# Performance work log

Hardware: AMD Instinct MI355X
Metric: run time of the kernel (lower is better)

## Reference

```python
import jax, jax.numpy as jnp
import numpy as np

N = 100_000            # nodes
E = 1_600_000          # edges per metapath
IN = 256               # input features
HEADS, DIM = 8, 16     # heads * dim = hidden_channels
HIDDEN = HEADS * DIM   # 128
OUT = 4                # classes
NEG_SLOPE = 0.2


def setup_inputs() -> dict:
    key = jax.random.key(0)
    ks = jax.random.split(key, 16)
    s = 1.0 / np.sqrt(HIDDEN)
    return {
        "x": jax.random.normal(ks[0], (N, IN), jnp.float32),
        "edge_index0": jax.random.randint(ks[1], (2, E), 0, N, jnp.int64),
        "edge_index1": jax.random.randint(ks[2], (2, E), 0, N, jnp.int64),
        "proj_w": jax.random.normal(ks[3], (IN, HIDDEN), jnp.float32) / np.sqrt(IN),
        "proj_b": jnp.zeros((HIDDEN,), jnp.float32),
        "att_src0": jax.random.normal(ks[4], (HEADS, DIM), jnp.float32) * s,
        "att_dst0": jax.random.normal(ks[5], (HEADS, DIM), jnp.float32) * s,
        "att_src1": jax.random.normal(ks[6], (HEADS, DIM), jnp.float32) * s,
        "att_dst1": jax.random.normal(ks[7], (HEADS, DIM), jnp.float32) * s,
        "k_lin_w": jax.random.normal(ks[8], (HIDDEN, HIDDEN), jnp.float32) * s,
        "k_lin_b": jnp.zeros((HIDDEN,), jnp.float32),
        "q": jax.random.normal(ks[9], (HIDDEN,), jnp.float32) * s,
        "lin_w": jax.random.normal(ks[10], (HIDDEN, OUT), jnp.float32) * s,
        "lin_b": jnp.zeros((OUT,), jnp.float32),
    }


def _metapath_conv(xp, a_src, a_dst, src, dst):
    # xp: [N,H,D]; a_src, a_dst: [H,D]; src/dst: [E]
    alpha_src = (xp * a_src).sum(-1)                     # [N,H]
    alpha_dst = (xp * a_dst).sum(-1)                     # [N,H]
    e = jax.nn.leaky_relu(alpha_src[src] + alpha_dst[dst], NEG_SLOPE)  # [E,H]
    emax = jax.ops.segment_max(e, dst, num_segments=N)  # [N,H] (stable softmax)
    e = jnp.exp(e - emax[dst])
    denom = jax.ops.segment_sum(e, dst, num_segments=N)
    alpha = e / (denom[dst] + 1e-16)                     # edge softmax per dst
    msg = xp[src] * alpha[..., None]                     # [E,H,D]
    out = jax.ops.segment_sum(msg, dst, num_segments=N)  # [N,H,D]
    return jax.nn.relu(out.reshape(N, HIDDEN))


def reference(x, edge_index0, edge_index1, proj_w, proj_b,
              att_src0, att_dst0, att_src1, att_dst1,
              k_lin_w, k_lin_b, q, lin_w, lin_b):
    # shared node-type projection
    xp = (x @ proj_w + proj_b).reshape(N, HEADS, DIM)
    # per-metapath GAT-style convolutions (dropout=0.6 is eval no-op)
    outs = jnp.stack([
        _metapath_conv(xp, att_src0, att_dst0, edge_index0[0], edge_index0[1]),
        _metapath_conv(xp, att_src1, att_dst1, edge_index1[0], edge_index1[1]),
    ])                                                    # [M,N,HIDDEN]
    # semantic attention over metapaths
    k = jnp.tanh(outs @ k_lin_w + k_lin_b).mean(axis=1)  # [M,HIDDEN]
    attn = jax.nn.softmax((k * q).sum(-1))               # [M]
    fused = (attn[:, None, None] * outs).sum(0)          # [N,HIDDEN]
    return fused @ lin_w + lin_b                          # [N,OUT]
```

## Files before the change

kernel.cpp:

```cpp
#include <hip/hip_runtime.h>
#include <hip/hip_bf16.h>

#define NN 100000
#define EE 1600000
#define HID 128
#define NEG 0.2f
#define CAP 64
#define BSH 9
#define NB 196
#define CAPB 9216
#define EBLK 4096
#define NBINB 391
#define NBUILD 392
#define NPROJ 512
#define NPREPW 208

typedef __attribute__((ext_vector_type(8))) short short8;
typedef __attribute__((ext_vector_type(4))) float f32x4;

static __device__ __forceinline__ float bf2f(short s) {
  union { float f; unsigned u; } c;
  c.u = ((unsigned)(unsigned short)s) << 16;
  return c.f;
}

static __device__ __forceinline__ float exp2_fast(float x) {
  float r;
  asm("v_exp_f32 %0, %1" : "=v"(r) : "v"(x));
  return r;
}

static __device__ __forceinline__ float tanh_fast(float x) {
  float a = fminf(fmaxf(x * 2.885390082f, -40.f), 40.f);
  float e = exp2_fast(a);
  float r = __builtin_amdgcn_rcpf(e + 1.f);
  return fmaf(-2.f, r, 1.f);
}

__global__ __launch_bounds__(256) void k_prep(const int* __restrict__ ei0,
    const int* __restrict__ ei1, const float* __restrict__ w,
    const float* __restrict__ kw,
    const float* __restrict__ a0s, const float* __restrict__ a0d,
    const float* __restrict__ a1s, const float* __restrict__ a1d,
    int* __restrict__ gcur, int* __restrict__ binned,
    short* __restrict__ wTg, short* __restrict__ kwTg, short* __restrict__ awTg) {
  const int bid = blockIdx.x;
  const int t = threadIdx.x;
  if (bid >= 2 * NBINB) {
    int i = (bid - 2 * NBINB) * 256 + t;
    if (i < 32768) {
      int n = i >> 8, k = i & 255;
      __hip_bfloat16 b = __float2bfloat16(w[k * 128 + n]);
      wTg[i] = *(short*)&b;
    } else if (i < 49152) {
      int j = i - 32768;
      int n = j >> 7, k = j & 127;
      __hip_bfloat16 b = __float2bfloat16(kw[k * 128 + n]);
      kwTg[j] = *(short*)&b;
    } else if (i < 53248) {
      int j = i - 49152;
      int c = j >> 7, k = j & 127;
      int p = c >> 4, dt = (c >> 3) & 1, h = c & 7;
      const float* arr = p ? (dt ? a1d : a1s) : (dt ? a0d : a0s);
      float v = ((k >> 4) == h) ? arr[h * 16 + (k & 15)] * 1.44269504f : 0.f;
      __hip_bfloat16 b = __float2bfloat16(v);
      awTg[j] = *(short*)&b;
    }
    return;
  }
  const int p = bid >= NBINB;
  const int bx = p ? bid - NBINB : bid;
  const int* __restrict__ ei = p ? ei1 : ei0;
  const int* __restrict__ src = ei;
  const int* __restrict__ dst = ei + EE;
  int* __restrict__ gc = gcur + p * 256;
  int* __restrict__ bn = binned + (size_t)p * NB * CAPB;
  __shared__ int cntL[NB], baseL[NB];
  const int e0 = bx * EBLK;
  const int e1 = min(e0 + EBLK, EE);
  for (int i = t; i < NB; i += 256) cntL[i] = 0;
  __syncthreads();
  int vj[16], bj[16];
#pragma unroll
  for (int j = 0; j < 16; j++) {
    int e = e0 + t + j * 256;
    bj[j] = -1;
    if (e < e1) {
      int d = dst[e];
      int b = d >> BSH;
      int off = atomicAdd(&cntL[b], 1);
      vj[j] = (src[e] << BSH) | (d & 511);
      bj[j] = (b << 14) | off;
    }
  }
  __syncthreads();
  for (int i = t; i < NB; i += 256) baseL[i] = atomicAdd(&gc[i], cntL[i]);
  __syncthreads();
#pragma unroll
  for (int j = 0; j < 16; j++) {
    if (bj[j] >= 0) {
      int b = bj[j] >> 14;
      int off = baseL[b] + (bj[j] & 16383);
      if (off < CAPB) bn[b * CAPB + off] = vj[j];
    }
  }
}

#define PWS 264
#define AWS 136
#define PNT ((NN + 15) / 16)

__global__ __launch_bounds__(512) void k_mid(
    const int* __restrict__ gcur, const int* __restrict__ binned,
    int* __restrict__ cnt, int* __restrict__ csr,
    const float* __restrict__ x, const short* __restrict__ wTg,
    const short* __restrict__ awTg, const float* __restrict__ bias,
    __hip_bfloat16* __restrict__ xph, float* __restrict__ alpha) {
  __shared__ short wT[128 * PWS];
  __shared__ short awT[32 * AWS];
  const int bid = blockIdx.x;
  const int tid = threadIdx.x;
  if (bid < NBUILD) {
    int* lc = (int*)wT;
    const int p = bid >= 196, b = p ? bid - 196 : bid;
    const int* __restrict__ bn = binned + (size_t)p * NB * CAPB + (size_t)b * CAPB;
    const int n = min(gcur[p * 256 + b], CAPB);
    int* __restrict__ cs = csr + (size_t)p * NN * CAP;
    lc[tid] = 0;
    __syncthreads();
    const int node0 = b << BSH;
    for (int i = tid; i < n; i += 512) {
      int v = bn[i];
      int ln = v & 511;
      int off = atomicAdd(&lc[ln], 1);
      if (off < CAP) cs[(size_t)(node0 + ln) * CAP + off] = v >> BSH;
    }
    __syncthreads();
    int n0 = node0 + tid;
    if (n0 < NN) cnt[p * NN + n0] = lc[tid];
    return;
  }
  const int pb = bid - NBUILD;
  for (int i = tid; i < 4096; i += 512) {
    int n = i >> 5, kc = i & 31;
    *(short8*)&wT[n * PWS + kc * 8] = *(const short8*)&wTg[n * 256 + kc * 8];
  }
  {
    int n = tid >> 4, kc = tid & 15;
    *(short8*)&awT[n * AWS + kc * 8] = *(const short8*)&awTg[n * 128 + kc * 8];
  }
  const int lane = tid & 63, wave = tid >> 6;
  const int rowgrp = lane >> 4, lcol = lane & 15;
  float bv[8];
#pragma unroll
  for (int ct = 0; ct < 8; ct++) bv[ct] = bias[ct * 16 + lcol];
  __syncthreads();
  short* __restrict__ xphS = (short*)xph;
  for (int tile = pb * 8 + wave; tile < PNT; tile += NPROJ * 8) {
    const int r0 = tile * 16;
    const float* xr = x + (size_t)(r0 + lcol) * 256 + rowgrp * 8;
    short8 af[8];
#pragma unroll
    for (int kc = 0; kc < 8; kc++) {
      float4 u0 = *(const float4*)(xr + kc * 32);
      float4 u1 = *(const float4*)(xr + kc * 32 + 4);
      union { short8 v; __hip_bfloat162 h[4]; } u;
      u.h[0] = __float22bfloat162_rn(make_float2(u0.x, u0.y));
      u.h[1] = __float22bfloat162_rn(make_float2(u0.z, u0.w));
      u.h[2] = __float22bfloat162_rn(make_float2(u1.x, u1.y));
      u.h[3] = __float22bfloat162_rn(make_float2(u1.z, u1.w));
      af[kc] = u.v;
    }
#pragma unroll
    for (int ct = 0; ct < 8; ct++) {
      f32x4 acc = {0.f, 0.f, 0.f, 0.f};
#pragma unroll
      for (int kc = 0; kc < 8; kc++) {
        short8 bf = *(const short8*)&wT[(ct * 16 + lcol) * PWS + kc * 32 + rowgrp * 8];
        acc = __builtin_amdgcn_mfma_f32_16x16x32_bf16(af[kc], bf, acc, 0, 0, 0);
      }
#pragma unroll
      for (int r = 0; r < 4; r++) {
        int orow = r0 + rowgrp * 4 + r;
        __hip_bfloat16 ob = __float2bfloat16(acc[r] + bv[ct]);
        xphS[(size_t)orow * 128 + ct * 16 + lcol] = *(short*)&ob;
      }
    }
    const short* xb = xphS + (size_t)(r0 + lcol) * 128 + rowgrp * 8;
    short8 af2[4];
#pragma unroll
    for (int kc = 0; kc < 4; kc++) af2[kc] = *(const short8*)(xb + kc * 32);
#pragma unroll
    for (int ct2 = 0; ct2 < 2; ct2++) {
      f32x4 acc2 = {0.f, 0.f, 0.f, 0.f};
#pragma unroll
      for (int kc = 0; kc < 4; kc++) {
        short8 bfa = *(const short8*)&awT[(ct2 * 16 + lcol) * AWS + kc * 32 + rowgrp * 8];
        acc2 = __builtin_amdgcn_mfma_f32_16x16x32_bf16(af2[kc], bfa, acc2, 0, 0, 0);
      }
#pragma unroll
      for (int r = 0; r < 4; r++)
        alpha[(size_t)(r0 + rowgrp * 4 + r) * 32 + ct2 * 16 + lcol] = acc2[r];
    }
  }
}


#define EDGE_BODY(sv)                                      \
  {                                                        \
    unsigned s = (unsigned)(sv);                           \
    float t = alpha[s * 32u + pofs + h];                   \
    __hip_bfloat162 v = xph[s * 64u + lane];               \
    float tt = t + ad;                                     \
    float al = exp2_fast(fmaxf(tt, NEG * tt));             \
    denom += al;                                           \
    float2 f = __bfloat1622float2(v);                      \
    a0 = fmaf(al, f.x, a0);                                \
    a1 = fmaf(al, f.y, a1);                                \
  }

__global__ __launch_bounds__(256) void k_aggr(const __hip_bfloat162* __restrict__ xph,
    const float* __restrict__ alpha,
    const int* __restrict__ cnt, const int* __restrict__ csr,
    __hip_bfloat162* __restrict__ h0, __hip_bfloat162* __restrict__ h1) {
  const int p = blockIdx.y;
  const unsigned lane = threadIdx.x & 63;
  int node = blockIdx.x * 4 + (threadIdx.x >> 6);
  if (node >= NN) return;
  node = __builtin_amdgcn_readfirstlane(node);
  const int* __restrict__ cs = csr + ((size_t)p * NN + node) * CAP;
  __hip_bfloat162* __restrict__ hout = p ? h1 : h0;
  const unsigned h = lane >> 3;
  const unsigned pofs = p * 16u;
  const float ad = alpha[(unsigned)node * 32u + pofs + 8u + h];
  const int deg = min(cnt[p * NN + node], CAP);

  float denom = 1e-16f, a0 = 0.f, a1 = 0.f;
  int e = 0;
  for (; e + 8 <= deg; e += 8) {
    int4 q0 = *(const int4*)&cs[e];
    int4 q1 = *(const int4*)&cs[e + 4];
    EDGE_BODY(q0.x) EDGE_BODY(q0.y) EDGE_BODY(q0.z) EDGE_BODY(q0.w)
    EDGE_BODY(q1.x) EDGE_BODY(q1.y) EDGE_BODY(q1.z) EDGE_BODY(q1.w)
  }
  for (; e + 4 <= deg; e += 4) {
    int4 q0 = *(const int4*)&cs[e];
    EDGE_BODY(q0.x) EDGE_BODY(q0.y) EDGE_BODY(q0.z) EDGE_BODY(q0.w)
  }
  for (; e < deg; e++) EDGE_BODY(cs[e])
  float inv = 1.f / denom;
  hout[(size_t)node * 64 + lane] =
      __float22bfloat162_rn(make_float2(fmaxf(a0 * inv, 0.f), fmaxf(a1 * inv, 0.f)));
}

#define KWS 136
#define NTILES ((NN + 63) / 64)
#define SEMGX 512

__global__ __launch_bounds__(256) void k_sem(const __hip_bfloat16* __restrict__ h0,
    const __hip_bfloat16* __restrict__ h1, const short* __restrict__ kwTg,
    const float* __restrict__ kb, const float* __restrict__ lw,
    float* __restrict__ ksum, float* __restrict__ o0, float* __restrict__ o1) {
  __shared__ short kwT[128 * KWS];
  __shared__ float red[4][128];
  __shared__ float lwS[512];
  const int tid = threadIdx.x;
  const int m = blockIdx.y;
  const short* __restrict__ hc = (const short*)(m ? h1 : h0);
  float* __restrict__ oc = m ? o1 : o0;
  for (int i = tid; i < 2048; i += 256) {
    int n = i >> 4, kc = i & 15;
    *(short8*)&kwT[n * KWS + kc * 8] = *(const short8*)&kwTg[n * 128 + kc * 8];
  }
  for (int l = tid; l < 512; l += 256) lwS[l] = lw[l];
  const int lane = tid & 63;
  const int wave = tid >> 6;
  const int rowgrp = lane >> 4;
  const int lcol = lane & 15;
  float partial[8] = {};
  float kbv[8];
#pragma unroll
  for (int ct = 0; ct < 8; ct++) kbv[ct] = kb[ct * 16 + lcol];
  __syncthreads();
  for (int tile = blockIdx.x; tile < NTILES; tile += SEMGX) {
    int n0 = tile * 64 + wave * 16;
    int row = n0 + lcol;
    if (row >= NN) row = 0;
    const short* hr = hc + (size_t)row * 128 + rowgrp * 8;
    short8 afrag[4];
#pragma unroll
    for (int kc = 0; kc < 4; kc++) afrag[kc] = *(const short8*)(hr + kc * 32);
    float op[4] = {0.f, 0.f, 0.f, 0.f};
#pragma unroll
    for (int kc = 0; kc < 4; kc++) {
      union { short8 v; short s[8]; } u;
      u.v = afrag[kc];
#pragma unroll
      for (int j = 0; j < 8; j++) {
        float hv = bf2f(u.s[j]);
        const float4 lv = *(const float4*)&lwS[(kc * 32 + rowgrp * 8 + j) * 4];
        op[0] = fmaf(hv, lv.x, op[0]);
        op[1] = fmaf(hv, lv.y, op[1]);
        op[2] = fmaf(hv, lv.z, op[2]);
        op[3] = fmaf(hv, lv.w, op[3]);
      }
    }
#pragma unroll
    for (int c = 0; c < 4; c++) {
      op[c] += __shfl_xor(op[c], 16, 64);
      op[c] += __shfl_xor(op[c], 32, 64);
    }
    int orow = n0 + lcol;
    if (rowgrp == 0 && orow < NN) {
      float4 ov = make_float4(op[0], op[1], op[2], op[3]);
      *(float4*)&oc[(size_t)orow * 4] = ov;
    }
#pragma unroll
    for (int ct = 0; ct < 8; ct++) {
      f32x4 acc = {0.f, 0.f, 0.f, 0.f};
#pragma unroll
      for (int kc = 0; kc < 4; kc++) {
        short8 bfrag = *(const short8*)&kwT[(ct * 16 + lcol) * KWS + kc * 32 + rowgrp * 8];
        acc = __builtin_amdgcn_mfma_f32_16x16x32_bf16(afrag[kc], bfrag, acc, 0, 0, 0);
      }
#pragma unroll
      for (int r = 0; r < 4; r++) {
        int node = n0 + rowgrp * 4 + r;
        if (node < NN) partial[ct] += tanh_fast(acc[r] + kbv[ct]);
      }
    }
  }
#pragma unroll
  for (int ct = 0; ct < 8; ct++) {
    partial[ct] += __shfl_xor(partial[ct], 16, 64);
    partial[ct] += __shfl_xor(partial[ct], 32, 64);
  }
  if (lane < 16) {
#pragma unroll
    for (int ct = 0; ct < 8; ct++) red[wave][ct * 16 + lane] = partial[ct];
  }
  __syncthreads();
  if (tid < 128) {
    float s = red[0][tid] + red[1][tid] + red[2][tid] + red[3][tid];
    atomicAdd(&ksum[m * 128 + tid], s);
  }
}

__global__ __launch_bounds__(256) void k_blend(const float* __restrict__ o0,
    const float* __restrict__ o1, const float* __restrict__ lb,
    const float* __restrict__ ksum, const float* __restrict__ q,
    float* __restrict__ out) {
  __shared__ float aw[2];
  const int t = threadIdx.x;
  if (t < 64) {
    float qa = q[t], qb = q[t + 64];
    float s0 = fmaf(ksum[t], qa, ksum[t + 64] * qb);
    float s1 = fmaf(ksum[128 + t], qa, ksum[192 + t] * qb);
#pragma unroll
    for (int off = 1; off < 64; off <<= 1) {
      s0 += __shfl_xor(s0, off, 64);
      s1 += __shfl_xor(s1, off, 64);
    }
    if (t == 0) {
      float l0 = s0 * (1.f / NN), l1 = s1 * (1.f / NN);
      float mx = fmaxf(l0, l1);
      float e0 = __expf(l0 - mx), e1 = __expf(l1 - mx);
      float inv = 1.f / (e0 + e1);
      aw[0] = e0 * inv;
      aw[1] = e1 * inv;
    }
  }
  __syncthreads();
  int i = blockIdx.x * 256 + t;
  if (i < NN * 4)
    out[i] = aw[0] * o0[i] + aw[1] * o1[i] + lb[i & 3];
}

extern "C" void kernel_launch(void* const* d_in, const int* in_sizes, int n_in,
                              void* d_out, int out_size, void* d_ws, size_t ws_size,
                              hipStream_t stream) {
  const float* x      = (const float*)d_in[0];
  const int*   ei0    = (const int*)d_in[1];
  const int*   ei1    = (const int*)d_in[2];
  const float* proj_w = (const float*)d_in[3];
  const float* proj_b = (const float*)d_in[4];
  const float* a0s    = (const float*)d_in[5];
  const float* a0d    = (const float*)d_in[6];
  const float* a1s    = (const float*)d_in[7];
  const float* a1d    = (const float*)d_in[8];
  const float* klw    = (const float*)d_in[9];
  const float* klb    = (const float*)d_in[10];
  const float* q      = (const float*)d_in[11];
  const float* lw     = (const float*)d_in[12];
  const float* lb     = (const float*)d_in[13];
  float* out = (float*)d_out;

  char* ws = (char*)d_ws;
  size_t off = 0;
  auto alloc = [&](size_t bytes) -> void* {
    size_t o = (off + 255) & ~(size_t)255;
    off = o + bytes;
    return (void*)(ws + o);
  };
  __hip_bfloat162* xph = (__hip_bfloat162*)alloc((size_t)NN * 128 * 2);
  __hip_bfloat162* h0  = (__hip_bfloat162*)alloc((size_t)NN * 128 * 2);
  __hip_bfloat162* h1  = (__hip_bfloat162*)alloc((size_t)NN * 128 * 2);
  float* alpha = (float*)alloc((size_t)NN * 32 * 4);
  float* ksum = (float*)alloc(256 * 4);
  int* gcur   = (int*)alloc(2 * 256 * 4);
  int* cnt    = (int*)alloc((size_t)2 * NN * 4);
  int* csr    = (int*)alloc((size_t)2 * NN * CAP * 4);
  int* binned = (int*)alloc((size_t)2 * NB * CAPB * 4);
  short* wTg  = (short*)alloc(32768 * 2);
  short* kwTg = (short*)alloc(16384 * 2);
  short* awTg = (short*)alloc(4096 * 2);
  float* o0   = (float*)alloc((size_t)NN * 4 * 4);
  float* o1   = (float*)alloc((size_t)NN * 4 * 4);

  hipMemsetAsync(ksum, 0, 256 * 4 + 2 * 256 * 4, stream);

  k_prep<<<dim3(2 * NBINB + NPREPW), 256, 0, stream>>>(ei0, ei1, proj_w, klw,
                                                       a0s, a0d, a1s, a1d,
                                                       gcur, binned, wTg, kwTg, awTg);
  k_mid<<<dim3(NBUILD + NPROJ), 512, 0, stream>>>(gcur, binned, cnt, csr,
                                                  x, wTg, awTg, proj_b,
                                                  (__hip_bfloat16*)xph, alpha);
  k_aggr<<<dim3((NN + 3) / 4, 2), 256, 0, stream>>>(xph, alpha, cnt, csr, h0, h1);
  k_sem<<<dim3(SEMGX, 2), 256, 0, stream>>>((const __hip_bfloat16*)h0,
                                            (const __hip_bfloat16*)h1, kwTg, klb, lw,
                                            ksum, o0, o1);
  k_blend<<<dim3((NN * 4 + 255) / 256), 256, 0, stream>>>(o0, o1, lb, ksum, q, out);
}
```

Measured before the change: 534.6 us.

## Stage CSR build in LDS with coalesced writeback and split alpha arrays

The CSR build now scatters neighbour ids into an LDS staging buffer in two half-bin passes, then copies whole 64-slot rows to global memory with coalesced int4 stores instead of scattered 4-byte writes. The CSR buffer is padded to the bin-aligned node count so the full-tile copy stays in bounds. The interleaved alpha array is split into four compact per-metapath src/dst arrays, so the gathered source scores in aggregation touch a denser 32-byte row per node. The cost is extra LDS passes and syncs in the build blocks, plus writing unused padded slots.

```diff
diff --git a/kernel.cpp b/kernel.cpp
--- a/kernel.cpp
+++ b/kernel.cpp
@@ -8,6 +8,7 @@
 #define CAP 64
 #define BSH 9
 #define NB 196
+#define NNP (NB * 512)
 #define CAPB 9216
 #define EBLK 4096
 #define NBINB 391
@@ -115,29 +116,42 @@
     int* __restrict__ cnt, int* __restrict__ csr,
     const float* __restrict__ x, const short* __restrict__ wTg,
     const short* __restrict__ awTg, const float* __restrict__ bias,
-    __hip_bfloat16* __restrict__ xph, float* __restrict__ alpha) {
+    __hip_bfloat16* __restrict__ xph,
+    float* __restrict__ as0, float* __restrict__ ad0,
+    float* __restrict__ as1, float* __restrict__ ad1) {
   __shared__ short wT[128 * PWS];
   __shared__ short awT[32 * AWS];
   const int bid = blockIdx.x;
   const int tid = threadIdx.x;
   if (bid < NBUILD) {
-    int* lc = (int*)wT;
+    int* stage = (int*)wT;
+    int* lc = (int*)awT;
     const int p = bid >= 196, b = p ? bid - 196 : bid;
     const int* __restrict__ bn = binned + (size_t)p * NB * CAPB + (size_t)b * CAPB;
     const int n = min(gcur[p * 256 + b], CAPB);
-    int* __restrict__ cs = csr + (size_t)p * NN * CAP;
-    lc[tid] = 0;
-    __syncthreads();
+    int* __restrict__ cs = csr + (size_t)p * NNP * CAP;
     const int node0 = b << BSH;
-    for (int i = tid; i < n; i += 512) {
-      int v = bn[i];
-      int ln = v & 511;
-      int off = atomicAdd(&lc[ln], 1);
-      if (off < CAP) cs[(size_t)(node0 + ln) * CAP + off] = v >> BSH;
-    }
-    __syncthreads();
-    int n0 = node0 + tid;
-    if (n0 < NN) cnt[p * NN + n0] = lc[tid];
+#pragma unroll 1
+    for (int half = 0; half < 2; half++) {
+      if (tid < 256) lc[tid] = 0;
+      __syncthreads();
+      for (int i = tid; i < n; i += 512) {
+        int v = bn[i];
+        int ln = v & 511;
+        if ((ln >> 8) == half) {
+          int lnh = ln & 255;
+          int off = atomicAdd(&lc[lnh], 1);
+          if (off < CAP) stage[lnh * CAP + off] = v >> BSH;
+        }
+      }
+      __syncthreads();
+      const int nodeH = node0 + half * 256;
+      int4* dst4 = (int4*)(cs + (size_t)nodeH * CAP);
+      const int4* src4 = (const int4*)stage;
+      for (int i = tid; i < 4096; i += 512) dst4[i] = src4[i];
+      if (tid < 256 && nodeH + tid < NN) cnt[p * NN + nodeH + tid] = lc[tid];
+      __syncthreads();
+    }
     return;
   }
   const int pb = bid - NBUILD;
@@ -151,6 +165,9 @@
   }
   const int lane = tid & 63, wave = tid >> 6;
   const int rowgrp = lane >> 4, lcol = lane & 15;
+  const int hh = lcol & 7;
+  float* __restrict__ apA = (lcol & 8) ? ad0 : as0;
+  float* __restrict__ apB = (lcol & 8) ? ad1 : as1;
   float bv[8];
 #pragma unroll
   for (int ct = 0; ct < 8; ct++) bv[ct] = bias[ct * 16 + lcol];
@@ -198,9 +215,10 @@
         short8 bfa = *(const short8*)&awT[(ct2 * 16 + lcol) * AWS + kc * 32 + rowgrp * 8];
         acc2 = __builtin_amdgcn_mfma_f32_16x16x32_bf16(af2[kc], bfa, acc2, 0, 0, 0);
       }
+      float* __restrict__ ap = ct2 ? apB : apA;
 #pragma unroll
       for (int r = 0; r < 4; r++)
-        alpha[(size_t)(r0 + rowgrp * 4 + r) * 32 + ct2 * 16 + lcol] = acc2[r];
+        ap[(size_t)(r0 + rowgrp * 4 + r) * 8 + hh] = acc2[r];
     }
   }
 }
@@ -209,7 +227,7 @@
 #define EDGE_BODY(sv)                                      \
   {                                                        \
     unsigned s = (unsigned)(sv);                           \
-    float t = alpha[s * 32u + pofs + h];                   \
+    float t = asrc[s * 8u + h];                            \
     __hip_bfloat162 v = xph[s * 64u + lane];               \
     float tt = t + ad;                                     \
     float al = exp2_fast(fmaxf(tt, NEG * tt));             \
@@ -220,7 +238,8 @@
   }
 
 __global__ __launch_bounds__(256) void k_aggr(const __hip_bfloat162* __restrict__ xph,
-    const float* __restrict__ alpha,
+    const float* __restrict__ as0, const float* __restrict__ ad0,
+    const float* __restrict__ as1, const float* __restrict__ ad1,
     const int* __restrict__ cnt, const int* __restrict__ csr,
     __hip_bfloat162* __restrict__ h0, __hip_bfloat162* __restrict__ h1) {
   const int p = blockIdx.y;
@@ -228,11 +247,12 @@
   int node = blockIdx.x * 4 + (threadIdx.x >> 6);
   if (node >= NN) return;
   node = __builtin_amdgcn_readfirstlane(node);
-  const int* __restrict__ cs = csr + ((size_t)p * NN + node) * CAP;
+  const float* __restrict__ asrc = p ? as1 : as0;
+  const float* __restrict__ adst = p ? ad1 : ad0;
+  const int* __restrict__ cs = csr + ((size_t)p * NNP + node) * CAP;
   __hip_bfloat162* __restrict__ hout = p ? h1 : h0;
   const unsigned h = lane >> 3;
-  const unsigned pofs = p * 16u;
-  const float ad = alpha[(unsigned)node * 32u + pofs + 8u + h];
+  const float ad = adst[(unsigned)node * 8u + h];
   const int deg = min(cnt[p * NN + node], CAP);
 
   float denom = 1e-16f, a0 = 0.f, a1 = 0.f;
@@ -405,11 +425,14 @@
   __hip_bfloat162* xph = (__hip_bfloat162*)alloc((size_t)NN * 128 * 2);
   __hip_bfloat162* h0  = (__hip_bfloat162*)alloc((size_t)NN * 128 * 2);
   __hip_bfloat162* h1  = (__hip_bfloat162*)alloc((size_t)NN * 128 * 2);
-  float* alpha = (float*)alloc((size_t)NN * 32 * 4);
+  float* as0  = (float*)alloc((size_t)NN * 8 * 4);
+  float* ad0  = (float*)alloc((size_t)NN * 8 * 4);
+  float* as1  = (float*)alloc((size_t)NN * 8 * 4);
+  float* ad1  = (float*)alloc((size_t)NN * 8 * 4);
   float* ksum = (float*)alloc(256 * 4);
   int* gcur   = (int*)alloc(2 * 256 * 4);
   int* cnt    = (int*)alloc((size_t)2 * NN * 4);
-  int* csr    = (int*)alloc((size_t)2 * NN * CAP * 4);
+  int* csr    = (int*)alloc((size_t)2 * NNP * CAP * 4);
   int* binned = (int*)alloc((size_t)2 * NB * CAPB * 4);
   short* wTg  = (short*)alloc(32768 * 2);
   short* kwTg = (short*)alloc(16384 * 2);
@@ -424,8 +447,10 @@
                                                        gcur, binned, wTg, kwTg, awTg);
   k_mid<<<dim3(NBUILD + NPROJ), 512, 0, stream>>>(gcur, binned, cnt, csr,
                                                   x, wTg, awTg, proj_b,
-                                                  (__hip_bfloat16*)xph, alpha);
-  k_aggr<<<dim3((NN + 3) / 4, 2), 256, 0, stream>>>(xph, alpha, cnt, csr, h0, h1);
+                                                  (__hip_bfloat16*)xph,
+                                                  as0, ad0, as1, ad1);
+  k_aggr<<<dim3((NN + 3) / 4, 2), 256, 0, stream>>>(xph, as0, ad0, as1, ad1,
+                                                    cnt, csr, h0, h1);
   k_sem<<<dim3(SEMGX, 2), 256, 0, stream>>>((const __hip_bfloat16*)h0,
                                             (const __hip_bfloat16*)h1, kwTg, klb, lw,
                                             ksum, o0, o1);
```

New measurement: 512.3 us. 1.04x faster.
